# Kernel optimization log

Measured on AMD Instinct MI355X. Metric: run time of the kernel, lower is better.

The kernel has to match this reference:

```python
import jax, jax.numpy as jnp
import numpy as np

E = 768      # embed_dim
H = 12       # num_heads
D = E // H   # head_dim = 64
G = 8        # num_groups (grouped 1x1 conv)
MAX_S = 197  # max_seq_len
RED = 8      # SE reduction ratio
S, B = 197, 64


def grouped_linear(x, w, b):
    """Grouped 1x1 conv as grouped linear. x: [..., Cin], w: [Cout, Cin//G], b: [Cout]."""
    cout = w.shape[0]
    cin = x.shape[-1]
    xg = x.reshape(x.shape[:-1] + (G, cin // G))
    wg = w.reshape(G, cout // G, cin // G)
    y = jnp.einsum('...gi,goi->...go', xg, wg)
    return y.reshape(x.shape[:-1] + (cout,)) + b


def channel_shuffle(x):
    """Shuffle channels (last dim) across G groups, matching torch channel_shuffle."""
    c = x.shape[-1]
    xg = x.reshape(x.shape[:-1] + (G, c // G))
    return jnp.swapaxes(xg, -1, -2).reshape(x.shape)


def layernorm(x, g, b, eps=1e-5):
    mu = jnp.mean(x, axis=-1, keepdims=True)
    var = jnp.var(x, axis=-1, keepdims=True)
    return (x - mu) * jax.lax.rsqrt(var + eps) * g + b


def setup_inputs() -> dict:
    rng = jax.random.key(0)
    ks = jax.random.split(rng, 16)
    std = 0.02
    return {
        'query': jax.random.normal(ks[0], (S, B, E), jnp.float32),
        'key':   jax.random.normal(ks[1], (S, B, E), jnp.float32),
        'value': jax.random.normal(ks[2], (S, B, E), jnp.float32),
        'qkv_w': jax.random.normal(ks[3], (3 * E, E // G), jnp.float32) * std,
        'qkv_b': jnp.zeros((3 * E,), jnp.float32),
        'out_w': jax.random.normal(ks[4], (E, E // G), jnp.float32) * std,
        'out_b': jnp.zeros((E,), jnp.float32),
        'rel_pos': jax.random.normal(ks[5], (2 * MAX_S - 1, D), jnp.float32) * std,
        'ln_g': jnp.ones((E,), jnp.float32),
        'ln_b': jnp.zeros((E,), jnp.float32),
        'fc1_w': jax.random.normal(ks[6], (E, E // RED), jnp.float32) * std,
        'fc1_b': jnp.zeros((E // RED,), jnp.float32),
        'fc2_w': jax.random.normal(ks[7], (E // RED, E), jnp.float32) * std,
        'fc2_b': jnp.zeros((E,), jnp.float32),
    }


def reference(query, key, value, qkv_w, qkv_b, out_w, out_b, rel_pos,
              ln_g, ln_b, fc1_w, fc1_b, fc2_w, fc2_b):
    seq_len, bsz, embed_dim = query.shape
    scaling = float(D) ** -0.5

    x = jnp.transpose(query, (1, 0, 2))              # [B, S, E]
    qkv = grouped_linear(x, qkv_w, qkv_b)            # [B, S, 3E]
    qkv = channel_shuffle(qkv)                       # [B, S, 3E]
    q, k, v = jnp.split(qkv, 3, axis=-1)             # each [B, S, E]

    def heads(t):                                    # [B, S, E] -> [B, H, S, D]
        return jnp.transpose(t.reshape(bsz, seq_len, H, D), (0, 2, 1, 3))
    q, k, v = heads(q) * scaling, heads(k), heads(v)

    attn_w = jnp.einsum('bhsd,bhtd->bhst', q, k)     # content-content

    # decoupled relative-position attention (note: slice, not skew, per source)
    rel = rel_pos[MAX_S - seq_len: MAX_S + seq_len - 1]           # [2S-1, D]
    content_pos = jnp.einsum('bhsd,rd->bhsr', q, rel)[..., seq_len - 1: 2 * seq_len - 1]
    pos_content = jnp.einsum('rd,bhtd->bhrt', rel, k)[:, :, seq_len - 1: 2 * seq_len - 1, :]
    attn_w = attn_w + content_pos + pos_content

    probs = jax.nn.softmax(attn_w, axis=-1)          # [B, H, S, S]
    attn = jnp.einsum('bhst,bhtd->bhsd', probs, v)   # [B, H, S, D]
    attn = jnp.transpose(attn, (0, 2, 1, 3)).reshape(bsz, seq_len, E)  # [B, S, E]

    # squeeze-excite style feature calibration gating
    scale = jax.nn.sigmoid(
        jnp.dot(jax.nn.gelu(jnp.dot(layernorm(attn, ln_g, ln_b), fc1_w) + fc1_b), fc2_w) + fc2_b)
    attn = attn * scale

    out = grouped_linear(attn, out_w, out_b)         # [B, S, E]
    out = jnp.transpose(out, (1, 0, 2))              # [S, B, E]

    avg_weights = jnp.sum(probs, axis=1) / H         # [B, S, S]
    return out, avg_weights
```

## Files before the change

kernel.cpp:

```cpp
#include <hip/hip_runtime.h>
#include <hip/hip_bf16.h>

constexpr int S = 197;
constexpr int B = 64;
constexpr int E = 768;
constexpr int H = 12;
constexpr int D = 64;
constexpr int M = S * B;
constexpr size_t SBE = (size_t)M * E;
constexpr int PST = 208;

typedef short bf16x8 __attribute__((ext_vector_type(8)));
typedef float f32x4 __attribute__((ext_vector_type(4)));
typedef unsigned int u32x4 __attribute__((ext_vector_type(4)));

__device__ __forceinline__ unsigned short f2b(float x) {
  unsigned int u = __float_as_uint(x);
  return (unsigned short)((u + 0x7FFFu + ((u >> 16) & 1u)) >> 16);
}
__device__ __forceinline__ float b2f(unsigned short u) {
  return __uint_as_float((unsigned int)u << 16);
}

__global__ __launch_bounds__(256) void mha_wprep(const float* __restrict__ w1,
                                                 const float* __restrict__ w2,
                                                 const float* __restrict__ lng,
                                                 const float* __restrict__ lnb,
                                                 const float* __restrict__ b1,
                                                 const float* __restrict__ rel,
                                                 const float* __restrict__ wq,
                                                 unsigned short* __restrict__ w1t,
                                                 unsigned short* __restrict__ w2t,
                                                 float* __restrict__ cgb,
                                                 float* __restrict__ cbb,
                                                 unsigned short* __restrict__ relb,
                                                 unsigned short* __restrict__ wqt) {
  const int bid = blockIdx.x, tid = threadIdx.x;
  if (bid < 288) {
    int idx = bid * 256 + tid;
    int n = idx / 768, k = idx - n * 768;
    w1t[idx] = f2b(lng[k] * w1[(size_t)k * 96 + n]);
  } else if (bid < 576) {
    int idx = (bid - 288) * 256 + tid;
    int n = idx / 96, k = idx - n * 96;
    w2t[idx] = f2b(w2[(size_t)k * 768 + n]);
  } else if (bid == 576) {
    if (tid < 96) {
      float cg = 0.f, cb = 0.f;
      for (int k = 0; k < 768; ++k) {
        float wv = w1[(size_t)k * 96 + tid];
        cg += lng[k] * wv;
        cb += lnb[k] * wv;
      }
      cgb[tid] = cg;
      cbb[tid] = cb + b1[tid];
    }
  } else if (bid < 641) {
    int idx = (bid - 577) * 256 + tid;
    int s2 = idx >> 6, d = idx & 63;
    float v = (s2 < S) ? rel[(size_t)(S - 1 + s2) * D + d] : 0.f;
    relb[idx] = f2b(v);
  } else {
    int idx = (bid - 641) * 256 + tid;
    wqt[idx] = f2b(wq[idx]);
  }
}

__global__ __launch_bounds__(256) void mha_xcvt(const float* __restrict__ x,
                                                unsigned short* __restrict__ xb) {
  size_t i = ((size_t)blockIdx.x * 256 + threadIdx.x) * 8;
  float4 v0 = *reinterpret_cast<const float4*>(x + i);
  float4 v1 = *reinterpret_cast<const float4*>(x + i + 4);
  unsigned short o[8] = {f2b(v0.x), f2b(v0.y), f2b(v0.z), f2b(v0.w),
                         f2b(v1.x), f2b(v1.y), f2b(v1.z), f2b(v1.w)};
  *(u32x4*)(xb + i) = *(const u32x4*)o;
}

__global__ __launch_bounds__(256) void mha_qkv_gemm(const unsigned short* __restrict__ xb,
                                                    const unsigned short* __restrict__ wqt,
                                                    const float* __restrict__ bias,
                                                    unsigned short* __restrict__ y) {
  const int m0 = blockIdx.x * 64;
  const int n0 = blockIdx.y * 96;
  const int g = blockIdx.y / 3;
  const int tid = threadIdx.x;
  const int lane = tid & 63, wv = tid >> 6;
  const int l15 = lane & 15, l4 = lane >> 4;

  const unsigned short* xr = xb + (size_t)(m0 + 16 * wv + l15) * E + g * 96 + l4 * 8;
  bf16x8 a0 = *(const bf16x8*)(xr);
  bf16x8 a1 = *(const bf16x8*)(xr + 32);
  bf16x8 a2 = *(const bf16x8*)(xr + 64);

  const int mloc = m0 + 16 * wv + 4 * l4;
#pragma unroll
  for (int nf = 0; nf < 6; ++nf) {
    const unsigned short* wr = wqt + (size_t)(n0 + nf * 16 + l15) * 96 + l4 * 8;
    f32x4 a = (f32x4){0.f, 0.f, 0.f, 0.f};
    a = __builtin_amdgcn_mfma_f32_16x16x32_bf16(a0, *(const bf16x8*)(wr), a, 0, 0, 0);
    a = __builtin_amdgcn_mfma_f32_16x16x32_bf16(a1, *(const bf16x8*)(wr + 32), a, 0, 0, 0);
    a = __builtin_amdgcn_mfma_f32_16x16x32_bf16(a2, *(const bf16x8*)(wr + 64), a, 0, 0, 0);
    int p = n0 + nf * 16 + l15;
    float bv = bias[p];
#pragma unroll
    for (int r = 0; r < 4; ++r)
      y[(size_t)(mloc + r) * 2304 + p] = f2b(a[r] + bv);
  }
}

__global__ __launch_bounds__(256) void mha_qkv_shuffle(const unsigned short* __restrict__ y,
                                                       const float* __restrict__ rel,
                                                       unsigned short* __restrict__ qb,
                                                       unsigned short* __restrict__ kb,
                                                       unsigned short* __restrict__ vb) {
  const int tid = threadIdx.x;
  const int lane = tid & 63;
  const int g = lane >> 3, j = lane & 7;
  const int d = j * 8 + g;
  const int wrow = tid >> 6;
  const int rbase = blockIdx.x * 16;

  float relv[4];
  int sA[4], bA[4];
#pragma unroll
  for (int r8 = 0; r8 < 4; ++r8) {
    int rowl = rbase + r8 * 4 + wrow;
    sA[r8] = rowl >> 6;
    bA[r8] = rowl & 63;
    relv[r8] = rel[(size_t)(S - 1 + sA[r8]) * D + d];
  }

  for (int h = 0; h < H; ++h) {
#pragma unroll
    for (int r8 = 0; r8 < 4; ++r8) {
      int rowl = rbase + r8 * 4 + wrow;
      const unsigned short* yr = y + (size_t)rowl * 2304 + g * 288 + h * 8 + j;
      size_t o = (((size_t)bA[r8] * H + h) * S + sA[r8]) * D + d;
      float vq = b2f(yr[0]);
      float vk = b2f(yr[96]);
      float vv = b2f(yr[192]);
      qb[o] = f2b(0.125f * vq + relv[r8]);
      kb[o] = f2b(vk + relv[r8]);
      vb[o] = f2b(vv);
    }
  }
}

__global__ __launch_bounds__(512) void mha_fattn(
    const unsigned short* __restrict__ qb, const unsigned short* __restrict__ kb,
    const unsigned short* __restrict__ vb, const unsigned short* __restrict__ relb,
    float* __restrict__ context, unsigned short* __restrict__ probs, int bh0) {
  __shared__ __align__(16) unsigned short KtPt[128 * 136];
  __shared__ __align__(16) unsigned short Vh[64 * 136];
  unsigned short* Kt = KtPt;
  unsigned short* Pt = KtPt;

  const int id = blockIdx.x;
  const int xcd = id & 7;
  const int rr = id >> 3;
  const int stile = rr & 1;
  const int bhl = xcd + 8 * (rr >> 1);
  const int bh = bh0 + bhl;
  const int b_ = bh / H, h_ = bh - b_ * H;
  const int s0 = stile * 128;
  const int tid = threadIdx.x;
  const int lane = tid & 63, w = tid >> 6;
  const int l15 = lane & 15, l4 = lane >> 4;
  const int vt = tid & 63;
  const int vdb = (tid >> 6) * 8;

  const unsigned short* qg = qb + (((size_t)bh * S + (s0 + 16 * w + l15)) << 6) + l4 * 8;
  const unsigned short* rg = relb + (((size_t)((s0 + 16 * w + l15) & 255)) << 6) + l4 * 8;
  bf16x8 aq0 = *(const bf16x8*)(qg);
  bf16x8 aq1 = *(const bf16x8*)(qg + 32);
  bf16x8 aq2 = *(const bf16x8*)(rg);
  bf16x8 aq3 = *(const bf16x8*)(rg + 32);

  const int kr = tid >> 3, kc = tid & 7;
  auto loadK = [&](int tc, u32x4& kv, u32x4& rv) {
    int tg = tc * 64 + kr;
    kv = (u32x4){0, 0, 0, 0};
    rv = (u32x4){0, 0, 0, 0};
    if (tg < S) {
      kv = *(const u32x4*)(kb + (((size_t)bh * S + tg) << 6) + kc * 8);
      u32x4 rvv = *(const u32x4*)(relb + ((size_t)tg << 6) + kc * 8);
      rv = rvv ^ 0x80008000u;
    }
  };

  f32x4 acc[13];
#pragma unroll
  for (int i = 0; i < 13; ++i) acc[i] = (f32x4){0.f, 0.f, 0.f, 0.f};

  u32x4 kvA, rvA, kvB, rvB;
  loadK(0, kvA, rvA);

#pragma unroll
  for (int tc = 0; tc < 4; ++tc) {
    u32x4 kvc = (tc & 1) ? kvB : kvA;
    u32x4 rvc = (tc & 1) ? rvB : rvA;
    *(u32x4*)(Kt + kr * 136 + kc * 8) = kvc;
    *(u32x4*)(Kt + kr * 136 + 64 + kc * 8) = rvc;
    if (tc < 3) {
      if (tc & 1) loadK(tc + 1, kvA, rvA);
      else        loadK(tc + 1, kvB, rvB);
    }
    __syncthreads();
#pragma unroll
    for (int tf = 0; tf < 4; ++tf) {
      if (tc == 3 && tf > 0) continue;
      const unsigned short* kbse = Kt + (tf * 16 + l15) * 136 + l4 * 8;
      f32x4 a = acc[tc * 4 + tf];
      a = __builtin_amdgcn_mfma_f32_16x16x32_bf16(aq0, *(const bf16x8*)(kbse), a, 0, 0, 0);
      a = __builtin_amdgcn_mfma_f32_16x16x32_bf16(aq1, *(const bf16x8*)(kbse + 32), a, 0, 0, 0);
      a = __builtin_amdgcn_mfma_f32_16x16x32_bf16(aq2, *(const bf16x8*)(kbse + 64), a, 0, 0, 0);
      a = __builtin_amdgcn_mfma_f32_16x16x32_bf16(aq3, *(const bf16x8*)(kbse + 96), a, 0, 0, 0);
      acc[tc * 4 + tf] = a;
    }
    __syncthreads();
  }

  u32x4 v1[2];
#pragma unroll
  for (int ii = 0; ii < 2; ++ii) {
    int t = ii * 64 + vt;
    v1[ii] = *(const u32x4*)(vb + (((size_t)bh * S + t) << 6) + vdb);
  }

  if (l15 >= 5) acc[12] = (f32x4){-3.0e38f, -3.0e38f, -3.0e38f, -3.0e38f};
  float inv[4];
#pragma unroll
  for (int r = 0; r < 4; ++r) {
    float m = acc[0][r];
#pragma unroll
    for (int tf = 1; tf < 13; ++tf) m = fmaxf(m, acc[tf][r]);
#pragma unroll
    for (int off = 1; off < 16; off <<= 1) m = fmaxf(m, __shfl_xor(m, off, 64));
    float s = 0.f;
#pragma unroll
    for (int tf = 0; tf < 13; ++tf) {
      float e = __expf(acc[tf][r] - m);
      acc[tf][r] = e;
      s += e;
    }
#pragma unroll
    for (int off = 1; off < 16; off <<= 1) s += __shfl_xor(s, off, 64);
    inv[r] = 1.f / s;
  }

  f32x4 ov[4];
#pragma unroll
  for (int df = 0; df < 4; ++df) ov[df] = (f32x4){0.f, 0.f, 0.f, 0.f};

#pragma unroll
  for (int tf = 0; tf < 8; ++tf)
#pragma unroll
    for (int r = 0; r < 4; ++r)
      Pt[(16 * w + 4 * l4 + r) * 136 + tf * 16 + l15] = f2b(acc[tf][r] * inv[r]);
#pragma unroll
  for (int ii = 0; ii < 2; ++ii) {
    int t = ii * 64 + vt;
    const unsigned short* vp = (const unsigned short*)&v1[ii];
#pragma unroll
    for (int j = 0; j < 8; ++j) Vh[(vdb + j) * 136 + t] = vp[j];
  }
  __syncthreads();

  u32x4 v2[2];
#pragma unroll
  for (int ii = 0; ii < 2; ++ii) {
    int t = 128 + ii * 64 + vt;
    v2[ii] = (u32x4){0, 0, 0, 0};
    if (t < S) v2[ii] = *(const u32x4*)(vb + (((size_t)bh * S + t) << 6) + vdb);
  }

  {
    const int r2 = tid >> 2;
    const int sg = s0 + r2;
    if (sg < S) {
#pragma unroll
      for (int j = 0; j < 4; ++j) {
        int c = (tid & 3) + 4 * j;
        u32x4 pv = *(const u32x4*)(Pt + r2 * 136 + c * 8);
        *(u32x4*)(probs + ((size_t)bhl * S + sg) * PST + c * 8) = pv;
      }
    }
  }
  {
    bf16x8 ap[4];
#pragma unroll
    for (int kf = 0; kf < 4; ++kf)
      ap[kf] = *(const bf16x8*)(Pt + (16 * w + l15) * 136 + kf * 32 + l4 * 8);
#pragma unroll
    for (int df = 0; df < 4; ++df) {
      const unsigned short* vbse = Vh + (df * 16 + l15) * 136 + l4 * 8;
      f32x4 o = ov[df];
#pragma unroll
      for (int kf = 0; kf < 4; ++kf)
        o = __builtin_amdgcn_mfma_f32_16x16x32_bf16(ap[kf], *(const bf16x8*)(vbse + kf * 32), o, 0, 0, 0);
      ov[df] = o;
    }
  }
  __syncthreads();

#pragma unroll
  for (int tf = 8; tf < 13; ++tf)
#pragma unroll
    for (int r = 0; r < 4; ++r)
      Pt[(16 * w + 4 * l4 + r) * 136 + (tf - 8) * 16 + l15] = f2b(acc[tf][r] * inv[r]);
#pragma unroll
  for (int r = 0; r < 4; ++r)
    Pt[(16 * w + 4 * l4 + r) * 136 + 80 + l15] = 0;
#pragma unroll
  for (int ii = 0; ii < 2; ++ii) {
    int t0h = ii * 64 + vt;
    if (t0h < 96) {
      const unsigned short* vp = (const unsigned short*)&v2[ii];
#pragma unroll
      for (int j = 0; j < 8; ++j) Vh[(vdb + j) * 136 + t0h] = vp[j];
    }
  }
  __syncthreads();

  {
    const int r2 = tid >> 2;
    const int sg = s0 + r2;
    if (sg < S) {
#pragma unroll
      for (int j = 0; j < 3; ++j) {
        int c = (tid & 3) + 4 * j;
        if (c < 10) {
          u32x4 pv = *(const u32x4*)(Pt + r2 * 136 + c * 8);
          *(u32x4*)(probs + ((size_t)bhl * S + sg) * PST + 128 + c * 8) = pv;
        }
      }
    }
  }
  {
    bf16x8 ap[3];
#pragma unroll
    for (int kf = 0; kf < 3; ++kf)
      ap[kf] = *(const bf16x8*)(Pt + (16 * w + l15) * 136 + kf * 32 + l4 * 8);
#pragma unroll
    for (int df = 0; df < 4; ++df) {
      const unsigned short* vbse = Vh + (df * 16 + l15) * 136 + l4 * 8;
      f32x4 o = ov[df];
#pragma unroll
      for (int kf = 0; kf < 3; ++kf)
        o = __builtin_amdgcn_mfma_f32_16x16x32_bf16(ap[kf], *(const bf16x8*)(vbse + kf * 32), o, 0, 0, 0);
      ov[df] = o;
    }
  }

#pragma unroll
  for (int df = 0; df < 4; ++df)
#pragma unroll
    for (int r = 0; r < 4; ++r) {
      int sg = s0 + 16 * w + 4 * l4 + r;
      if (sg < S)
        context[((size_t)b_ * S + sg) * E + h_ * 64 + df * 16 + l15] = ov[df][r];
    }
}

__global__ __launch_bounds__(256) void mha_avgred(const unsigned short* __restrict__ probs,
                                                  float* __restrict__ avg, int b0) {
  const int bs = blockIdx.x;
  const int bl = bs / S, s = bs - bl * S;
  const int t = threadIdx.x;
  if (t >= S) return;
  float acc = 0.f;
#pragma unroll
  for (int h = 0; h < H; ++h)
    acc += b2f(probs[(((size_t)bl * H + h) * S + s) * PST + t]);
  avg[(((size_t)(b0 + bl)) * S + s) * S + t] = acc * (1.f / H);
}

__global__ __launch_bounds__(128) void mha_fc1ln(const float* __restrict__ ctx,
                                                 const unsigned short* __restrict__ w1t,
                                                 const float* __restrict__ cgb,
                                                 const float* __restrict__ cbb,
                                                 unsigned short* __restrict__ h1) {
  __shared__ __align__(16) unsigned short As[32 * 104];
  __shared__ __align__(16) unsigned short Wl[48 * 104];
  __shared__ float smu[32], sinv[32];
  const int m0 = blockIdx.x * 32;
  const int n0 = blockIdx.y * 48;
  const int tid = threadIdx.x;
  const int lane = tid & 63, w = tid >> 6;
  const int l15 = lane & 15, l4 = lane >> 4;
  const int r = tid >> 2, q = tid & 3;

  float s1 = 0.f, s2 = 0.f;
  f32x4 acc[3];
#pragma unroll
  for (int nf = 0; nf < 3; ++nf) acc[nf] = (f32x4){0.f, 0.f, 0.f, 0.f};

  for (int c = 0; c < 8; ++c) {
    const int k0 = c * 96;
    {
      const float* xr = ctx + (size_t)(m0 + r) * E + k0 + q * 24;
      unsigned short* ar = As + r * 104 + q * 24;
#pragma unroll
      for (int j = 0; j < 6; ++j) {
        float4 v = *reinterpret_cast<const float4*>(xr + j * 4);
        s1 += v.x + v.y + v.z + v.w;
        s2 += v.x * v.x + v.y * v.y + v.z * v.z + v.w * v.w;
        ar[j * 4 + 0] = f2b(v.x); ar[j * 4 + 1] = f2b(v.y);
        ar[j * 4 + 2] = f2b(v.z); ar[j * 4 + 3] = f2b(v.w);
      }
    }
    for (int i = tid; i < 48 * 12; i += 128) {
      int n = i / 12, c8 = i - n * 12;
      *(u32x4*)(Wl + n * 104 + c8 * 8) =
          *(const u32x4*)(w1t + (size_t)(n0 + n) * E + k0 + c8 * 8);
    }
    __syncthreads();
    const unsigned short* arow = As + (16 * w + l15) * 104 + l4 * 8;
    bf16x8 a0 = *(const bf16x8*)(arow);
    bf16x8 a1 = *(const bf16x8*)(arow + 32);
    bf16x8 a2 = *(const bf16x8*)(arow + 64);
#pragma unroll
    for (int nf = 0; nf < 3; ++nf) {
      const unsigned short* wr = Wl + (nf * 16 + l15) * 104 + l4 * 8;
      f32x4 a = acc[nf];
      a = __builtin_amdgcn_mfma_f32_16x16x32_bf16(a0, *(const bf16x8*)(wr), a, 0, 0, 0);
      a = __builtin_amdgcn_mfma_f32_16x16x32_bf16(a1, *(const bf16x8*)(wr + 32), a, 0, 0, 0);
      a = __builtin_amdgcn_mfma_f32_16x16x32_bf16(a2, *(const bf16x8*)(wr + 64), a, 0, 0, 0);
      acc[nf] = a;
    }
    __syncthreads();
  }

  s1 += __shfl_xor(s1, 1, 64); s1 += __shfl_xor(s1, 2, 64);
  s2 += __shfl_xor(s2, 1, 64); s2 += __shfl_xor(s2, 2, 64);
  if (q == 0) {
    float mu = s1 * (1.f / E);
    float var = s2 * (1.f / E) - mu * mu;
    smu[r] = mu;
    sinv[r] = rsqrtf(var + 1e-5f);
  }
  __syncthreads();

#pragma unroll
  for (int nf = 0; nf < 3; ++nf) {
    int n = n0 + nf * 16 + l15;
    float cg = cgb[n], cb = cbb[n];
#pragma unroll
    for (int rr = 0; rr < 4; ++rr) {
      int ml = 16 * w + 4 * l4 + rr;
      float u = sinv[ml] * (acc[nf][rr] - smu[ml] * cg) + cb;
      float gl = 0.5f * u * (1.f + tanhf(0.7978845608028654f * (u + 0.044715f * u * u * u)));
      h1[(size_t)(m0 + ml) * 96 + n] = f2b(gl);
    }
  }
}

__global__ __launch_bounds__(256) void mha_fc2(const unsigned short* __restrict__ h1,
                                               const unsigned short* __restrict__ w2t,
                                               const float* __restrict__ bias,
                                               const float* __restrict__ ctx,
                                               unsigned short* __restrict__ attn2) {
  __shared__ __align__(16) unsigned short Hs[64 * 104];
  __shared__ __align__(16) unsigned short Wl[192 * 104];
  const int m0 = blockIdx.x * 64;
  const int n0 = blockIdx.y * 192;
  const int tid = threadIdx.x;
  const int lane = tid & 63, w = tid >> 6;
  const int l15 = lane & 15, l4 = lane >> 4;

  for (int i = tid; i < 64 * 12; i += 256) {
    int rr = i / 12, c8 = i - rr * 12;
    *(u32x4*)(Hs + rr * 104 + c8 * 8) =
        *(const u32x4*)(h1 + (size_t)(m0 + rr) * 96 + c8 * 8);
  }
  for (int i = tid; i < 192 * 12; i += 256) {
    int n = i / 12, c8 = i - n * 12;
    *(u32x4*)(Wl + n * 104 + c8 * 8) =
        *(const u32x4*)(w2t + (size_t)(n0 + n) * 96 + c8 * 8);
  }
  __syncthreads();

  const unsigned short* arow = Hs + (16 * w + l15) * 104 + l4 * 8;
  bf16x8 a0 = *(const bf16x8*)(arow);
  bf16x8 a1 = *(const bf16x8*)(arow + 32);
  bf16x8 a2 = *(const bf16x8*)(arow + 64);

#pragma unroll
  for (int nf = 0; nf < 12; ++nf) {
    const unsigned short* wr = Wl + (nf * 16 + l15) * 104 + l4 * 8;
    f32x4 a = (f32x4){0.f, 0.f, 0.f, 0.f};
    a = __builtin_amdgcn_mfma_f32_16x16x32_bf16(a0, *(const bf16x8*)(wr), a, 0, 0, 0);
    a = __builtin_amdgcn_mfma_f32_16x16x32_bf16(a1, *(const bf16x8*)(wr + 32), a, 0, 0, 0);
    a = __builtin_amdgcn_mfma_f32_16x16x32_bf16(a2, *(const bf16x8*)(wr + 64), a, 0, 0, 0);
    int n = n0 + nf * 16 + l15;
    float bv = bias[n];
#pragma unroll
    for (int rr = 0; rr < 4; ++rr) {
      int m = m0 + 16 * w + 4 * l4 + rr;
      float val = a[rr] + bv;
      float sg = 1.f / (1.f + __expf(-val));
      float cv = ctx[(size_t)m * E + n];
      attn2[(size_t)m * E + n] = f2b(cv * sg);
    }
  }
}

__global__ __launch_bounds__(256) void mha_out(const unsigned short* __restrict__ attn2,
                                               const float* __restrict__ w,
                                               const float* __restrict__ bias,
                                               float* __restrict__ outp) {
  __shared__ __align__(16) unsigned short Asl[64 * 104];
  __shared__ __align__(16) unsigned short Wl[96 * 104];
  __shared__ float bias_s[96];
  const int m0 = blockIdx.x * 64;
  const int g = blockIdx.y;
  const int n0 = g * 96;
  const int tid = threadIdx.x;
  const int lane = tid & 63, w_ = tid >> 6;
  const int l15 = lane & 15, l4 = lane >> 4;

  for (int i = tid; i < 64 * 12; i += 256) {
    int rr = i / 12, c8 = i - rr * 12;
    *(u32x4*)(Asl + rr * 104 + c8 * 8) =
        *(const u32x4*)(attn2 + (size_t)(m0 + rr) * E + n0 + c8 * 8);
  }
  for (int i = tid; i < 96 * 24; i += 256) {
    int n = i / 24, c4 = i - n * 24;
    float4 v = *reinterpret_cast<const float4*>(&w[(size_t)(n0 + n) * 96 + c4 * 4]);
    unsigned short* dst = Wl + n * 104 + c4 * 4;
    dst[0] = f2b(v.x); dst[1] = f2b(v.y); dst[2] = f2b(v.z); dst[3] = f2b(v.w);
  }
  if (tid < 96) bias_s[tid] = bias[n0 + tid];
  __syncthreads();

  const unsigned short* arow = Asl + (16 * w_ + l15) * 104 + l4 * 8;
  bf16x8 a0 = *(const bf16x8*)(arow);
  bf16x8 a1 = *(const bf16x8*)(arow + 32);
  bf16x8 a2 = *(const bf16x8*)(arow + 64);

  int bb4[4], ss4[4];
#pragma unroll
  for (int rr = 0; rr < 4; ++rr) {
    int m = m0 + 16 * w_ + 4 * l4 + rr;
    bb4[rr] = m / S;
    ss4[rr] = m - bb4[rr] * S;
  }

#pragma unroll
  for (int nf = 0; nf < 6; ++nf) {
    const unsigned short* wr = Wl + (nf * 16 + l15) * 104 + l4 * 8;
    f32x4 a = (f32x4){0.f, 0.f, 0.f, 0.f};
    a = __builtin_amdgcn_mfma_f32_16x16x32_bf16(a0, *(const bf16x8*)(wr), a, 0, 0, 0);
    a = __builtin_amdgcn_mfma_f32_16x16x32_bf16(a1, *(const bf16x8*)(wr + 32), a, 0, 0, 0);
    a = __builtin_amdgcn_mfma_f32_16x16x32_bf16(a2, *(const bf16x8*)(wr + 64), a, 0, 0, 0);
    int p = n0 + nf * 16 + l15;
    float bv = bias_s[p - n0];
#pragma unroll
    for (int rr = 0; rr < 4; ++rr)
      outp[((size_t)ss4[rr] * B + bb4[rr]) * E + p] = a[rr] + bv;
  }
}

extern "C" void kernel_launch(void* const* d_in, const int* in_sizes, int n_in,
                              void* d_out, int out_size, void* d_ws, size_t ws_size,
                              hipStream_t stream) {
  const float* query = (const float*)d_in[0];
  const float* qkv_w = (const float*)d_in[3];
  const float* qkv_b = (const float*)d_in[4];
  const float* out_w = (const float*)d_in[5];
  const float* out_b = (const float*)d_in[6];
  const float* rel   = (const float*)d_in[7];
  const float* ln_g  = (const float*)d_in[8];
  const float* ln_b  = (const float*)d_in[9];
  const float* fc1_w = (const float*)d_in[10];
  const float* fc1_b = (const float*)d_in[11];
  const float* fc2_w = (const float*)d_in[12];
  const float* fc2_b = (const float*)d_in[13];

  float* ws = (float*)d_ws;
  unsigned short* qb   = (unsigned short*)ws;
  unsigned short* xbuf = qb;
  unsigned short* kbuf = qb + SBE;
  unsigned short* vbb  = kbuf + SBE;
  unsigned short* relb = vbb + SBE;
  size_t off = 3 * SBE / 2 + 8192;
  float* context = ws + off;
  unsigned short* attn2b = (unsigned short*)(ws + off + SBE);
  unsigned short* ybuf = (unsigned short*)context;
  unsigned short* h1b = attn2b + SBE;
  unsigned short* w1t = h1b + (size_t)M * 96;
  unsigned short* w2t = w1t + 73728;
  unsigned short* wqt = w2t + 73728;
  float* cgb = (float*)(wqt + 221184);
  float* cbb = cgb + 96;
  unsigned short* probsb = (unsigned short*)(cbb + 96);
  float* outp = (float*)d_out;
  float* avgp = outp + SBE;

  size_t used_f = off + SBE + (SBE + (size_t)M * 96 + 368640) / 2 + 192;
  size_t avail_f = (ws_size / 4 > used_f) ? ws_size / 4 - used_f : 0;
  int Bc = 2;
  const int cand[6] = {64, 32, 16, 8, 4, 2};
  for (int i = 0; i < 6; ++i) {
    size_t need_f = ((size_t)cand[i] * H * S * PST + 1) / 2;
    if (need_f <= avail_f) { Bc = cand[i]; break; }
  }

  mha_wprep<<<1505, 256, 0, stream>>>(fc1_w, fc2_w, ln_g, ln_b, fc1_b, rel, qkv_w,
                                      w1t, w2t, cgb, cbb, relb, wqt);
  mha_xcvt<<<(int)(SBE / 8 / 256), 256, 0, stream>>>(query, xbuf);

  mha_qkv_gemm<<<dim3(M / 64, 24), 256, 0, stream>>>(xbuf, wqt, qkv_b, ybuf);
  mha_qkv_shuffle<<<M / 16, 256, 0, stream>>>(ybuf, rel, qb, kbuf, vbb);

  for (int b0 = 0; b0 < B; b0 += Bc) {
    int bc = (B - b0 < Bc) ? (B - b0) : Bc;
    int nbh = bc * H;
    mha_fattn<<<2 * nbh, 512, 0, stream>>>(qb, kbuf, vbb, relb, context, probsb,
                                           b0 * H);
    mha_avgred<<<bc * S, 256, 0, stream>>>(probsb, avgp, b0);
  }

  mha_fc1ln<<<dim3(M / 32, 2), 128, 0, stream>>>(context, w1t, cgb, cbb, h1b);
  mha_fc2<<<dim3(M / 64, 4), 256, 0, stream>>>(h1b, w2t, fc2_b, context, attn2b);
  mha_out<<<dim3(M / 64, 8), 256, 0, stream>>>(attn2b, out_w, out_b, outp);
}
```

Before: 259.2 us.

## Fuse input conversion into QKV GEMM, store bf16 context, double-buffer K tiles

Removes the separate fp32-to-bf16 conversion kernel: the QKV GEMM now reads fp32 query directly and converts in registers. The attention context is written as bf16 rather than fp32, which halves the traffic for the context write and for its reads in the fc1/layernorm and fc2 gating kernels. In the attention kernel the K/rel tile goes into two alternating shared-memory buffers, dropping one barrier per chunk so the next tile's stores overlap the current MFMAs. The trade-off is lower-precision context feeding layernorm statistics and gating, and the GEMM now reads twice the input bytes across its 24 column blocks.

```diff
diff --git a/kernel.cpp b/kernel.cpp
--- a/kernel.cpp
+++ b/kernel.cpp
@@ -66,17 +66,7 @@
   }
 }
 
-__global__ __launch_bounds__(256) void mha_xcvt(const float* __restrict__ x,
-                                                unsigned short* __restrict__ xb) {
-  size_t i = ((size_t)blockIdx.x * 256 + threadIdx.x) * 8;
-  float4 v0 = *reinterpret_cast<const float4*>(x + i);
-  float4 v1 = *reinterpret_cast<const float4*>(x + i + 4);
-  unsigned short o[8] = {f2b(v0.x), f2b(v0.y), f2b(v0.z), f2b(v0.w),
-                         f2b(v1.x), f2b(v1.y), f2b(v1.z), f2b(v1.w)};
-  *(u32x4*)(xb + i) = *(const u32x4*)o;
-}
-
-__global__ __launch_bounds__(256) void mha_qkv_gemm(const unsigned short* __restrict__ xb,
+__global__ __launch_bounds__(256) void mha_qkv_gemm(const float* __restrict__ x,
                                                     const unsigned short* __restrict__ wqt,
                                                     const float* __restrict__ bias,
                                                     unsigned short* __restrict__ y) {
@@ -87,10 +77,17 @@
   const int lane = tid & 63, wv = tid >> 6;
   const int l15 = lane & 15, l4 = lane >> 4;
 
-  const unsigned short* xr = xb + (size_t)(m0 + 16 * wv + l15) * E + g * 96 + l4 * 8;
-  bf16x8 a0 = *(const bf16x8*)(xr);
-  bf16x8 a1 = *(const bf16x8*)(xr + 32);
-  bf16x8 a2 = *(const bf16x8*)(xr + 64);
+  const float* xr = x + (size_t)(m0 + 16 * wv + l15) * E + g * 96 + l4 * 8;
+  auto ldfrag = [](const float* p) -> bf16x8 {
+    float4 u = *reinterpret_cast<const float4*>(p);
+    float4 v = *reinterpret_cast<const float4*>(p + 4);
+    unsigned short t[8] = {f2b(u.x), f2b(u.y), f2b(u.z), f2b(u.w),
+                           f2b(v.x), f2b(v.y), f2b(v.z), f2b(v.w)};
+    return *(const bf16x8*)t;
+  };
+  bf16x8 a0 = ldfrag(xr);
+  bf16x8 a1 = ldfrag(xr + 32);
+  bf16x8 a2 = ldfrag(xr + 64);
 
   const int mloc = m0 + 16 * wv + 4 * l4;
 #pragma unroll
@@ -149,7 +146,7 @@
 __global__ __launch_bounds__(512) void mha_fattn(
     const unsigned short* __restrict__ qb, const unsigned short* __restrict__ kb,
     const unsigned short* __restrict__ vb, const unsigned short* __restrict__ relb,
-    float* __restrict__ context, unsigned short* __restrict__ probs, int bh0) {
+    unsigned short* __restrict__ ctxb, unsigned short* __restrict__ probs, int bh0) {
   __shared__ __align__(16) unsigned short KtPt[128 * 136];
   __shared__ __align__(16) unsigned short Vh[64 * 136];
   unsigned short* Kt = KtPt;
@@ -194,22 +191,27 @@
 
   u32x4 kvA, rvA, kvB, rvB;
   loadK(0, kvA, rvA);
+  *(u32x4*)(Kt + kr * 136 + kc * 8) = kvA;
+  *(u32x4*)(Kt + kr * 136 + 64 + kc * 8) = rvA;
+  loadK(1, kvB, rvB);
+  __syncthreads();
 
 #pragma unroll
   for (int tc = 0; tc < 4; ++tc) {
-    u32x4 kvc = (tc & 1) ? kvB : kvA;
-    u32x4 rvc = (tc & 1) ? rvB : rvA;
-    *(u32x4*)(Kt + kr * 136 + kc * 8) = kvc;
-    *(u32x4*)(Kt + kr * 136 + 64 + kc * 8) = rvc;
+    const int boff = (tc & 1) * 64 * 136;
     if (tc < 3) {
-      if (tc & 1) loadK(tc + 1, kvA, rvA);
-      else        loadK(tc + 1, kvB, rvB);
-    }
-    __syncthreads();
+      u32x4 skv = (tc & 1) ? kvA : kvB;
+      u32x4 srv = (tc & 1) ? rvA : rvB;
+      const int sboff = ((tc + 1) & 1) * 64 * 136;
+      *(u32x4*)(Kt + sboff + kr * 136 + kc * 8) = skv;
+      *(u32x4*)(Kt + sboff + kr * 136 + 64 + kc * 8) = srv;
+      if (tc == 0) loadK(2, kvA, rvA);
+      else if (tc == 1) loadK(3, kvB, rvB);
+    }
 #pragma unroll
     for (int tf = 0; tf < 4; ++tf) {
       if (tc == 3 && tf > 0) continue;
-      const unsigned short* kbse = Kt + (tf * 16 + l15) * 136 + l4 * 8;
+      const unsigned short* kbse = Kt + boff + (tf * 16 + l15) * 136 + l4 * 8;
       f32x4 a = acc[tc * 4 + tf];
       a = __builtin_amdgcn_mfma_f32_16x16x32_bf16(aq0, *(const bf16x8*)(kbse), a, 0, 0, 0);
       a = __builtin_amdgcn_mfma_f32_16x16x32_bf16(aq1, *(const bf16x8*)(kbse + 32), a, 0, 0, 0);
@@ -358,7 +360,7 @@
     for (int r = 0; r < 4; ++r) {
       int sg = s0 + 16 * w + 4 * l4 + r;
       if (sg < S)
-        context[((size_t)b_ * S + sg) * E + h_ * 64 + df * 16 + l15] = ov[df][r];
+        ctxb[((size_t)b_ * S + sg) * E + h_ * 64 + df * 16 + l15] = f2b(ov[df][r]);
     }
 }
 
@@ -375,7 +377,7 @@
   avg[(((size_t)(b0 + bl)) * S + s) * S + t] = acc * (1.f / H);
 }
 
-__global__ __launch_bounds__(128) void mha_fc1ln(const float* __restrict__ ctx,
+__global__ __launch_bounds__(128) void mha_fc1ln(const unsigned short* __restrict__ ctxb,
                                                  const unsigned short* __restrict__ w1t,
                                                  const float* __restrict__ cgb,
                                                  const float* __restrict__ cbb,
@@ -398,15 +400,20 @@
   for (int c = 0; c < 8; ++c) {
     const int k0 = c * 96;
     {
-      const float* xr = ctx + (size_t)(m0 + r) * E + k0 + q * 24;
+      const unsigned short* xr = ctxb + (size_t)(m0 + r) * E + k0 + q * 24;
+      unsigned short loc[24];
+      *(u32x4*)(loc) = *(const u32x4*)(xr);
+      *(u32x4*)(loc + 8) = *(const u32x4*)(xr + 8);
+      *(u32x4*)(loc + 16) = *(const u32x4*)(xr + 16);
       unsigned short* ar = As + r * 104 + q * 24;
-#pragma unroll
-      for (int j = 0; j < 6; ++j) {
-        float4 v = *reinterpret_cast<const float4*>(xr + j * 4);
-        s1 += v.x + v.y + v.z + v.w;
-        s2 += v.x * v.x + v.y * v.y + v.z * v.z + v.w * v.w;
-        ar[j * 4 + 0] = f2b(v.x); ar[j * 4 + 1] = f2b(v.y);
-        ar[j * 4 + 2] = f2b(v.z); ar[j * 4 + 3] = f2b(v.w);
+      *(u32x4*)(ar) = *(const u32x4*)(loc);
+      *(u32x4*)(ar + 8) = *(const u32x4*)(loc + 8);
+      *(u32x4*)(ar + 16) = *(const u32x4*)(loc + 16);
+#pragma unroll
+      for (int j = 0; j < 24; ++j) {
+        float v = b2f(loc[j]);
+        s1 += v;
+        s2 += v * v;
       }
     }
     for (int i = tid; i < 48 * 12; i += 128) {
@@ -458,7 +465,7 @@
 __global__ __launch_bounds__(256) void mha_fc2(const unsigned short* __restrict__ h1,
                                                const unsigned short* __restrict__ w2t,
                                                const float* __restrict__ bias,
-                                               const float* __restrict__ ctx,
+                                               const unsigned short* __restrict__ ctxb,
                                                unsigned short* __restrict__ attn2) {
   __shared__ __align__(16) unsigned short Hs[64 * 104];
   __shared__ __align__(16) unsigned short Wl[192 * 104];
@@ -499,7 +506,7 @@
       int m = m0 + 16 * w + 4 * l4 + rr;
       float val = a[rr] + bv;
       float sg = 1.f / (1.f + __expf(-val));
-      float cv = ctx[(size_t)m * E + n];
+      float cv = b2f(ctxb[(size_t)m * E + n]);
       attn2[(size_t)m * E + n] = f2b(cv * sg);
     }
   }
@@ -579,12 +586,12 @@
 
   float* ws = (float*)d_ws;
   unsigned short* qb   = (unsigned short*)ws;
-  unsigned short* xbuf = qb;
   unsigned short* kbuf = qb + SBE;
   unsigned short* vbb  = kbuf + SBE;
   unsigned short* relb = vbb + SBE;
   size_t off = 3 * SBE / 2 + 8192;
   float* context = ws + off;
+  unsigned short* ctxb = (unsigned short*)context;
   unsigned short* attn2b = (unsigned short*)(ws + off + SBE);
   unsigned short* ybuf = (unsigned short*)context;
   unsigned short* h1b = attn2b + SBE;
@@ -608,20 +615,19 @@
 
   mha_wprep<<<1505, 256, 0, stream>>>(fc1_w, fc2_w, ln_g, ln_b, fc1_b, rel, qkv_w,
                                       w1t, w2t, cgb, cbb, relb, wqt);
-  mha_xcvt<<<(int)(SBE / 8 / 256), 256, 0, stream>>>(query, xbuf);
-
-  mha_qkv_gemm<<<dim3(M / 64, 24), 256, 0, stream>>>(xbuf, wqt, qkv_b, ybuf);
+
+  mha_qkv_gemm<<<dim3(M / 64, 24), 256, 0, stream>>>(query, wqt, qkv_b, ybuf);
   mha_qkv_shuffle<<<M / 16, 256, 0, stream>>>(ybuf, rel, qb, kbuf, vbb);
 
   for (int b0 = 0; b0 < B; b0 += Bc) {
     int bc = (B - b0 < Bc) ? (B - b0) : Bc;
     int nbh = bc * H;
-    mha_fattn<<<2 * nbh, 512, 0, stream>>>(qb, kbuf, vbb, relb, context, probsb,
+    mha_fattn<<<2 * nbh, 512, 0, stream>>>(qb, kbuf, vbb, relb, ctxb, probsb,
                                            b0 * H);
     mha_avgred<<<bc * S, 256, 0, stream>>>(probsb, avgp, b0);
   }
 
-  mha_fc1ln<<<dim3(M / 32, 2), 128, 0, stream>>>(context, w1t, cgb, cbb, h1b);
-  mha_fc2<<<dim3(M / 64, 4), 256, 0, stream>>>(h1b, w2t, fc2_b, context, attn2b);
+  mha_fc1ln<<<dim3(M / 32, 2), 128, 0, stream>>>(ctxb, w1t, cgb, cbb, h1b);
+  mha_fc2<<<dim3(M / 64, 4), 256, 0, stream>>>(h1b, w2t, fc2_b, ctxb, attn2b);
   mha_out<<<dim3(M / 64, 8), 256, 0, stream>>>(attn2b, out_w, out_b, outp);
 }
```

After: 247.9 us. 1.05x faster.
